# Kernel optimization log

Hardware: AMD Instinct MI355X
Metric: run time of the kernel (lower is better)

Reference implementation:

```python
import jax, jax.numpy as jnp
import numpy as np

NUM_HEADS = 4
ALPHA = 0.2  # LeakyReLU negative slope


def setup_inputs() -> dict:
    key = jax.random.key(0)
    k1, k2 = jax.random.split(key)
    input_tensor = jax.random.normal(k1, (2, 4096, 128), dtype=jnp.float32)
    adj_matrix = jax.random.randint(k2, (4096, 4096), 0, 2, dtype=jnp.int32)
    return {"input_tensor": input_tensor, "adj_matrix": adj_matrix}


def reference(input_tensor, adj_matrix):
    B, S, F = input_tensor.shape
    H = NUM_HEADS
    x = input_tensor.reshape(B, S, H, F // H)          # (B,S,H,K)
    # full dense score matrix, QK^T-like with shared projection (identity)
    scores = jnp.einsum('bihk,bjhk->bhij', x, x)        # (B,H,S,S)
    scores = jax.nn.leaky_relu(scores, negative_slope=ALPHA)
    # adjacency mask broadcast over (B,H)
    scores = jnp.where(adj_matrix[None, None, :, :] == 0, -jnp.inf, scores)
    probs = jax.nn.softmax(scores, axis=-1)             # dropout p=0 -> identity
    out = jnp.einsum('bhij,bjhk->bihk', probs, x)       # (B,S,H,K)
    return out.reshape(B, S, F)                          # concat=True
```

## Files before the change

### kernel.cpp

```cpp
#include <hip/hip_runtime.h>
#include <stdint.h>

#define SEQ 4096
#define FDIM 128
#define NH 4
#define HD 32
#define NB 2
#define NROWS (NB * NH * SEQ)
#define LOG2E 1.4426950408889634f
#define VCOL 72
#define VHALF (32 * VCOL)

typedef float f32x4 __attribute__((ext_vector_type(4)));
typedef float f32x2 __attribute__((ext_vector_type(2)));
typedef __bf16 bf16x8 __attribute__((ext_vector_type(8)));

__device__ __forceinline__ unsigned short f2bf(float f) {
  unsigned int u = __builtin_bit_cast(unsigned int, f);
  return (unsigned short)((u + 0x7FFFu + ((u >> 16) & 1u)) >> 16);
}

__global__ void cvt_kernel(const float* __restrict__ in, unsigned short* __restrict__ out) {
  int i = (blockIdx.x * 256 + threadIdx.x) * 4;
  float4 v = *reinterpret_cast<const float4*>(in + i);
  ushort4 o;
  o.x = f2bf(v.x); o.y = f2bf(v.y); o.z = f2bf(v.z); o.w = f2bf(v.w);
  *reinterpret_cast<ushort4*>(out + i) = o;
}

__global__ void adjpack_kernel(const int* __restrict__ adj, unsigned short* __restrict__ bits16) {
  size_t t = (size_t)blockIdx.x * 256 + threadIdx.x;
  const uint4* p = reinterpret_cast<const uint4*>(adj) + t * 4;
  uint4 a = p[0], b = p[1], c = p[2], d = p[3];
  unsigned m = 0;
  m |= (a.x != 0) ? 1u : 0u;        m |= (a.y != 0) ? 2u : 0u;
  m |= (a.z != 0) ? 4u : 0u;        m |= (a.w != 0) ? 8u : 0u;
  m |= (b.x != 0) ? 16u : 0u;       m |= (b.y != 0) ? 32u : 0u;
  m |= (b.z != 0) ? 64u : 0u;       m |= (b.w != 0) ? 128u : 0u;
  m |= (c.x != 0) ? 256u : 0u;      m |= (c.y != 0) ? 512u : 0u;
  m |= (c.z != 0) ? 1024u : 0u;     m |= (c.w != 0) ? 2048u : 0u;
  m |= (d.x != 0) ? 4096u : 0u;     m |= (d.y != 0) ? 8192u : 0u;
  m |= (d.z != 0) ? 16384u : 0u;    m |= (d.w != 0) ? 32768u : 0u;
  bits16[t] = (unsigned short)m;
}

#define STEP(T, RB, WBUF)                                                       \
  {                                                                             \
    __syncthreads();                                                            \
    const bool pfok = (T) + 1 < NT;                                             \
    if (pfok) {      \
      sptr += 64 * FDIM;                                                        \
      r0 = *reinterpret_cast<const uint2*>(sptr);                               \
      r1 = *reinterpret_cast<const uint2*>(sptr + FDIM);                        \
      wnext = brow[bcol0 + (T) + 1];                                            \
    }                                                                           \
    f32x4 sc[4];                                                                \
    __builtin_amdgcn_s_setprio(1);                                              \
    _Pragma("unroll") for (int t4 = 0; t4 < 4; ++t4) {                          \
      bf16x8 kf = __builtin_bit_cast(bf16x8,                                    \
          *reinterpret_cast<const uint4*>(&Kl[RB][t4 * 16 + ql][g * 8]));       \
      sc[t4] = __builtin_amdgcn_mfma_f32_16x16x32_bf16(kf, qf, zf, 0, 0, 0);    \
    }                                                                           \
    __builtin_amdgcn_s_setprio(0);                                              \
    const unsigned long long wsh = wcur >> (4 * g);                             \
    const int mwl = (int)(unsigned)wsh, mwh = (int)(unsigned)(wsh >> 32);       \
    float pf4[4][4];                                                            \
    _Pragma("unroll") for (int t4 = 0; t4 < 4; ++t4) {                          \
      const int word = (t4 & 2) ? mwh : mwl;                                    \
      f32x2 lo = {sc[t4][0], sc[t4][1]}, hi = {sc[t4][2], sc[t4][3]};           \
      f32x2 lo2, hi2;                                                           \
      asm("v_pk_mul_f32 %0, %1, %2" : "=v"(lo2) : "v"(lo), "v"(p02));           \
      asm("v_pk_mul_f32 %0, %1, %2" : "=v"(hi2) : "v"(hi), "v"(p02));           \
      _Pragma("unroll") for (int r = 0; r < 4; ++r) {                           \
        const float alt = (r < 2) ? lo2[r & 1] : hi2[r & 1];                    \
        const float v = fmaxf(sc[t4][r], alt);                  \
        const float e = __builtin_amdgcn_exp2f(v);          \
        const int msk = __builtin_amdgcn_sbfe(word, 16 * (t4 & 1) + r, 1);      \
        pf4[t4][r] = __builtin_bit_cast(                                        \
            float, __builtin_bit_cast(unsigned, e) & (unsigned)msk);            \
      }                                                                         \
    }                                                                           \
    __builtin_amdgcn_s_setprio(1);                                              \
    _Pragma("unroll") for (int u = 0; u < 2; ++u) {                             \
      bf16x8 pa;                                                                \
      _Pragma("unroll") for (int tp = 0; tp < 2; ++tp)                          \
          _Pragma("unroll") for (int r = 0; r < 4; ++r)                         \
              pa[tp * 4 + r] = (__bf16)pf4[2 * u + tp][r];                      \
      bf16x8 vf0 = __builtin_bit_cast(bf16x8,                                   \
          *reinterpret_cast<const uint4*>(&Vp[RB][ql * VCOL + u * 32 + g * 8]));        \
      bf16x8 vf1 = __builtin_bit_cast(bf16x8,                                   \
          *reinterpret_cast<const uint4*>(&Vp[RB][(16 + ql) * VCOL + u * 32 + g * 8])); \
      acc0 = __builtin_amdgcn_mfma_f32_16x16x32_bf16(pa, vf0, acc0, 0, 0, 0);   \
      acc1 = __builtin_amdgcn_mfma_f32_16x16x32_bf16(pa, vf1, acc1, 0, 0, 0);   \
      accL = __builtin_amdgcn_mfma_f32_16x16x32_bf16(pa, ones, accL, 0, 0, 0);  \
    }                                                                           \
    __builtin_amdgcn_s_setprio(0);                                              \
    if (pfok) {   \
      *reinterpret_cast<uint2*>(&Kl[WBUF][2 * pr][c4 * 4]) = r0;                \
      *reinterpret_cast<uint2*>(&Kl[WBUF][2 * pr + 1][c4 * 4]) = r1;            \
      unsigned* vw = reinterpret_cast<unsigned*>(&Vp[WBUF][0]) + pi0h;          \
      vw[(4 * c4 + 0) * 36] = __builtin_amdgcn_perm(r1.x, r0.x, selA);          \
      vw[(4 * c4 + 1) * 36] = __builtin_amdgcn_perm(r1.x, r0.x, selB);          \
      vw[(4 * c4 + 2) * 36] = __builtin_amdgcn_perm(r1.y, r0.y, selA);          \
      vw[(4 * c4 + 3) * 36] = __builtin_amdgcn_perm(r1.y, r0.y, selB);          \
    }                                                                           \
    wcur = wnext;                                                               \
  }

template <int NSPLIT>
__global__ __launch_bounds__(256, 4) void gat_kernel(
    const unsigned short* __restrict__ xbf,
    const unsigned long long* __restrict__ bits,
    float* __restrict__ dst,
    float* __restrict__ lbuf) {
  __shared__ __align__(16) unsigned short Kl[2][64][40];
  __shared__ __align__(16) unsigned short Vp[2][VHALF];

  const int bh = blockIdx.y;
  const int b = bh >> 2;
  const int h = bh & 3;
  const int tid = threadIdx.x;
  const int wid = tid >> 6;
  const int lane = tid & 63;
  const int g = lane >> 4;
  const int ql = lane & 15;
  const int qw = blockIdx.x * 64 + wid * 16;
  const int jbase = blockIdx.z * (SEQ / NSPLIT);
  const int NT = (SEQ / NSPLIT) / 64;

  const unsigned short* xb = xbf + ((size_t)b * SEQ) * FDIM + h * HD;

  bf16x8 qraw = __builtin_bit_cast(bf16x8,
      *reinterpret_cast<const uint4*>(xb + (size_t)(qw + ql) * FDIM + g * 8));
  bf16x8 qf;
#pragma unroll
  for (int e = 0; e < 8; ++e) qf[e] = (__bf16)((float)qraw[e] * LOG2E);

  bf16x8 ones;
#pragma unroll
  for (int e = 0; e < 8; ++e) ones[e] = (__bf16)1.0f;
  const f32x4 zf = {0.f, 0.f, 0.f, 0.f};
  const f32x2 p02 = {0.2f, 0.2f};

  f32x4 acc0 = {0.f, 0.f, 0.f, 0.f};
  f32x4 acc1 = {0.f, 0.f, 0.f, 0.f};
  f32x4 accL = {0.f, 0.f, 0.f, 0.f};

  const unsigned long long* brow = bits + (size_t)(qw + ql) * (SEQ / 64);
  const int bcol0 = jbase >> 6;

  const int pr = tid >> 3;
  const int c4 = tid & 7;
  const unsigned short* sptr = xb + (size_t)(jbase + 2 * pr) * FDIM + c4 * 4;

  const int pi0h =
      (32 * (pr >> 4) + 8 * ((pr >> 1) & 3) + 4 * ((pr >> 3) & 1) + 2 * (pr & 1)) >> 1;

  const unsigned selA = 0x05040100u;
  const unsigned selB = 0x07060302u;

  uint2 r0 = *reinterpret_cast<const uint2*>(sptr);
  uint2 r1 = *reinterpret_cast<const uint2*>(sptr + FDIM);
  unsigned long long wcur = brow[bcol0];
  unsigned long long wnext = 0;
  *reinterpret_cast<uint2*>(&Kl[0][2 * pr][c4 * 4]) = r0;
  *reinterpret_cast<uint2*>(&Kl[0][2 * pr + 1][c4 * 4]) = r1;
  {
    unsigned* vw = reinterpret_cast<unsigned*>(&Vp[0][0]) + pi0h;
    vw[(4 * c4 + 0) * 36] = __builtin_amdgcn_perm(r1.x, r0.x, selA);
    vw[(4 * c4 + 1) * 36] = __builtin_amdgcn_perm(r1.x, r0.x, selB);
    vw[(4 * c4 + 2) * 36] = __builtin_amdgcn_perm(r1.y, r0.y, selA);
    vw[(4 * c4 + 3) * 36] = __builtin_amdgcn_perm(r1.y, r0.y, selB);
  }

  for (int t = 0; t < NT; t += 2) {
    STEP(t, 0, 1);
    STEP(t + 1, 1, 0);
  }

  if (NSPLIT == 1) {
#pragma unroll
    for (int r = 0; r < 4; ++r) {
      const float inv = 1.f / accL[r];
      const size_t o = ((size_t)b * SEQ + (size_t)(qw + 4 * g + r)) * FDIM + h * HD;
      dst[o + ql] = acc0[r] * inv;
      dst[o + 16 + ql] = acc1[r] * inv;
    }
  } else {
    float* Op = dst + (((size_t)blockIdx.z * (NB * NH) + bh) * SEQ) * HD;
#pragma unroll
    for (int r = 0; r < 4; ++r) {
      const int q = qw + 4 * g + r;
      Op[(size_t)q * HD + ql] = acc0[r];
      Op[(size_t)q * HD + 16 + ql] = acc1[r];
    }
    if (ql == 0) {
#pragma unroll
      for (int r = 0; r < 4; ++r)
        lbuf[(size_t)blockIdx.z * NROWS + (size_t)bh * SEQ + qw + 4 * g + r] = accL[r];
    }
  }
}

template <int NSPLIT>
__global__ __launch_bounds__(256) void combine_kernel(
    const float* __restrict__ Op, const float* __restrict__ lbuf, float* __restrict__ out) {
  const int idx = blockIdx.x * 256 + threadIdx.x;
  const int row = idx >> 3;
  const int dc = (idx & 7) * 4;
  float lt = 0.f;
  float4 o = {0.f, 0.f, 0.f, 0.f};
#pragma unroll
  for (int s = 0; s < NSPLIT; ++s) {
    lt += lbuf[(size_t)s * NROWS + row];
    float4 v = *reinterpret_cast<const float4*>(Op + ((size_t)s * NROWS + row) * HD + dc);
    o.x += v.x; o.y += v.y; o.z += v.z; o.w += v.w;
  }
  const float inv = 1.f / lt;
  const int bh = row >> 12;
  const int q = row & (SEQ - 1);
  const int b = bh >> 2;
  const int h = bh & 3;
  float4 w;
  w.x = o.x * inv; w.y = o.y * inv; w.z = o.z * inv; w.w = o.w * inv;
  *reinterpret_cast<float4*>(out + ((size_t)b * SEQ + q) * FDIM + h * HD + dc) = w;
}

extern "C" void kernel_launch(void* const* d_in, const int* in_sizes, int n_in,
                              void* d_out, int out_size, void* d_ws, size_t ws_size,
                              hipStream_t stream) {
  (void)in_sizes; (void)n_in; (void)out_size;
  const float* x = (const float*)d_in[0];
  const int* adj = (const int*)d_in[1];
  float* outp = (float*)d_out;

  unsigned short* xbf = (unsigned short*)d_ws;
  unsigned short* bits16 = (unsigned short*)((char*)d_ws + (2u << 20));
  float* Opart = (float*)((char*)d_ws + (4u << 20));
  auto need = [](int s) {
    return (size_t)(4u << 20) + (size_t)s * NROWS * HD * 4 + (size_t)s * NROWS * 4;
  };

  cvt_kernel<<<(NB * SEQ * FDIM) / (256 * 4), 256, 0, stream>>>(x, xbf);
  adjpack_kernel<<<(SEQ * SEQ) / (16 * 256), 256, 0, stream>>>(adj, bits16);

  const unsigned long long* bits = (const unsigned long long*)bits16;
  if (ws_size >= need(4)) {
    float* mlb = (float*)((char*)d_ws + (4u << 20) + (size_t)4 * NROWS * HD * 4);
    dim3 grid(SEQ / 64, NB * NH, 4);
    gat_kernel<4><<<grid, 256, 0, stream>>>(xbf, bits, Opart, mlb);
    combine_kernel<4><<<(NROWS * 8) / 256, 256, 0, stream>>>(Opart, mlb, outp);
  } else if (ws_size >= need(2)) {
    float* mlb = (float*)((char*)d_ws + (4u << 20) + (size_t)2 * NROWS * HD * 4);
    dim3 grid(SEQ / 64, NB * NH, 2);
    gat_kernel<2><<<grid, 256, 0, stream>>>(xbf, bits, Opart, mlb);
    combine_kernel<2><<<(NROWS * 8) / 256, 256, 0, stream>>>(Opart, mlb, outp);
  } else {
    dim3 grid(SEQ / 64, NB * NH, 1);
    gat_kernel<1><<<grid, 256, 0, stream>>>(xbf, bits, outp, nullptr);
  }
}
```

Baseline: 75.88 us.

## Process two 16-query tiles per wave to reuse shared K/V fragments

Each wave now handles 32 query rows (two 16-row MFMA tiles) instead of 16, so every K and V fragment loaded from shared memory feeds twice as many MFMAs and the per-block staging of K/V tiles covers 128 queries. The grid shrinks by half in x. The leaky-relu is rewritten as a scalar fmaxf(v, 0.2v) instead of packed multiplies. The cost is roughly double accumulator and score registers per thread, which may lower occupancy under launch_bounds(256,4), and half as many blocks for the GPU to spread across its compute units.

Result: faster. 71.13 us (-6.3%).

```diff
diff --git a/kernel.cpp b/kernel.cpp
--- a/kernel.cpp
+++ b/kernel.cpp
@@ -12,7 +12,6 @@
 #define VHALF (32 * VCOL)
 
 typedef float f32x4 __attribute__((ext_vector_type(4)));
-typedef float f32x2 __attribute__((ext_vector_type(2)));
 typedef __bf16 bf16x8 __attribute__((ext_vector_type(8)));
 
 __device__ __forceinline__ unsigned short f2bf(float f) {
@@ -44,6 +43,29 @@
   bits16[t] = (unsigned short)m;
 }
 
+#define SOFTMAX_HALF(SC, WC, PA0, PA1)                                          \
+  {                                                                             \
+    const unsigned long long wsh = (WC) >> (4 * g);                             \
+    const int mwl = (int)(unsigned)wsh, mwh = (int)(unsigned)(wsh >> 32);       \
+    float pf4[4][4];                                                            \
+    _Pragma("unroll") for (int t4 = 0; t4 < 4; ++t4) {                          \
+      const int word = (t4 & 2) ? mwh : mwl;                                    \
+      _Pragma("unroll") for (int r = 0; r < 4; ++r) {                           \
+        float v = SC[t4][r];                                                    \
+        v = fmaxf(v, 0.2f * v);                                 \
+        float e = __builtin_amdgcn_exp2f(v);                \
+        const int msk = __builtin_amdgcn_sbfe(word, 16 * (t4 & 1) + r, 1);      \
+        pf4[t4][r] = __builtin_bit_cast(                                        \
+            float, __builtin_bit_cast(unsigned, e) & (unsigned)msk);            \
+      }                                                                         \
+    }                                                                           \
+    _Pragma("unroll") for (int tp = 0; tp < 2; ++tp)                            \
+        _Pragma("unroll") for (int r = 0; r < 4; ++r) {                         \
+          PA0[tp * 4 + r] = (__bf16)pf4[tp][r];                                 \
+          PA1[tp * 4 + r] = (__bf16)pf4[2 + tp][r];                             \
+        }                                                                       \
+  }
+
 #define STEP(T, RB, WBUF)                                                       \
   {                                                                             \
     __syncthreads();                                                            \
@@ -52,48 +74,45 @@
       sptr += 64 * FDIM;                                                        \
       r0 = *reinterpret_cast<const uint2*>(sptr);                               \
       r1 = *reinterpret_cast<const uint2*>(sptr + FDIM);                        \
-      wnext = brow[bcol0 + (T) + 1];                                            \
-    }                                                                           \
-    f32x4 sc[4];                                                                \
+      wnA = browA[bcol0 + (T) + 1];                                             \
+      wnB = browB[bcol0 + (T) + 1];                                             \
+    }                                                                           \
+                     \
+    bf16x8 kf[4];                                                               \
+    _Pragma("unroll") for (int t4 = 0; t4 < 4; ++t4)                            \
+        kf[t4] = __builtin_bit_cast(bf16x8,                                     \
+            *reinterpret_cast<const uint4*>(&Kl[RB][t4 * 16 + ql][g * 8]));     \
+    bf16x8 vf0 = __builtin_bit_cast(bf16x8,                                     \
+        *reinterpret_cast<const uint4*>(&Vp[RB][ql * VCOL + g * 8]));           \
+    bf16x8 vf1 = __builtin_bit_cast(bf16x8,                                     \
+        *reinterpret_cast<const uint4*>(&Vp[RB][(16 + ql) * VCOL + g * 8]));    \
+    bf16x8 vf2 = __builtin_bit_cast(bf16x8,                                     \
+        *reinterpret_cast<const uint4*>(&Vp[RB][ql * VCOL + 32 + g * 8]));      \
+    bf16x8 vf3 = __builtin_bit_cast(bf16x8,                                     \
+        *reinterpret_cast<const uint4*>(&Vp[RB][(16 + ql) * VCOL + 32 + g * 8])); \
+    f32x4 scA[4], scB[4];                                                       \
     __builtin_amdgcn_s_setprio(1);                                              \
     _Pragma("unroll") for (int t4 = 0; t4 < 4; ++t4) {                          \
-      bf16x8 kf = __builtin_bit_cast(bf16x8,                                    \
-          *reinterpret_cast<const uint4*>(&Kl[RB][t4 * 16 + ql][g * 8]));       \
-      sc[t4] = __builtin_amdgcn_mfma_f32_16x16x32_bf16(kf, qf, zf, 0, 0, 0);    \
+      scA[t4] = __builtin_amdgcn_mfma_f32_16x16x32_bf16(kf[t4], qfA, zf, 0, 0, 0); \
+      scB[t4] = __builtin_amdgcn_mfma_f32_16x16x32_bf16(kf[t4], qfB, zf, 0, 0, 0); \
     }                                                                           \
     __builtin_amdgcn_s_setprio(0);                                              \
-    const unsigned long long wsh = wcur >> (4 * g);                             \
-    const int mwl = (int)(unsigned)wsh, mwh = (int)(unsigned)(wsh >> 32);       \
-    float pf4[4][4];                                                            \
-    _Pragma("unroll") for (int t4 = 0; t4 < 4; ++t4) {                          \
-      const int word = (t4 & 2) ? mwh : mwl;                                    \
-      f32x2 lo = {sc[t4][0], sc[t4][1]}, hi = {sc[t4][2], sc[t4][3]};           \
-      f32x2 lo2, hi2;                                                           \
-      asm("v_pk_mul_f32 %0, %1, %2" : "=v"(lo2) : "v"(lo), "v"(p02));           \
-      asm("v_pk_mul_f32 %0, %1, %2" : "=v"(hi2) : "v"(hi), "v"(p02));           \
-      _Pragma("unroll") for (int r = 0; r < 4; ++r) {                           \
-        const float alt = (r < 2) ? lo2[r & 1] : hi2[r & 1];                    \
-        const float v = fmaxf(sc[t4][r], alt);                  \
-        const float e = __builtin_amdgcn_exp2f(v);          \
-        const int msk = __builtin_amdgcn_sbfe(word, 16 * (t4 & 1) + r, 1);      \
-        pf4[t4][r] = __builtin_bit_cast(                                        \
-            float, __builtin_bit_cast(unsigned, e) & (unsigned)msk);            \
-      }                                                                         \
-    }                                                                           \
+    bf16x8 paA0, paA1, paB0, paB1;                                              \
+    SOFTMAX_HALF(scA, wcA, paA0, paA1);                                         \
+    SOFTMAX_HALF(scB, wcB, paB0, paB1);                                         \
     __builtin_amdgcn_s_setprio(1);                                              \
-    _Pragma("unroll") for (int u = 0; u < 2; ++u) {                             \
-      bf16x8 pa;                                                                \
-      _Pragma("unroll") for (int tp = 0; tp < 2; ++tp)                          \
-          _Pragma("unroll") for (int r = 0; r < 4; ++r)                         \
-              pa[tp * 4 + r] = (__bf16)pf4[2 * u + tp][r];                      \
-      bf16x8 vf0 = __builtin_bit_cast(bf16x8,                                   \
-          *reinterpret_cast<const uint4*>(&Vp[RB][ql * VCOL + u * 32 + g * 8]));        \
-      bf16x8 vf1 = __builtin_bit_cast(bf16x8,                                   \
-          *reinterpret_cast<const uint4*>(&Vp[RB][(16 + ql) * VCOL + u * 32 + g * 8])); \
-      acc0 = __builtin_amdgcn_mfma_f32_16x16x32_bf16(pa, vf0, acc0, 0, 0, 0);   \
-      acc1 = __builtin_amdgcn_mfma_f32_16x16x32_bf16(pa, vf1, acc1, 0, 0, 0);   \
-      accL = __builtin_amdgcn_mfma_f32_16x16x32_bf16(pa, ones, accL, 0, 0, 0);  \
-    }                                                                           \
+    accA0 = __builtin_amdgcn_mfma_f32_16x16x32_bf16(paA0, vf0, accA0, 0, 0, 0); \
+    accA1 = __builtin_amdgcn_mfma_f32_16x16x32_bf16(paA0, vf1, accA1, 0, 0, 0); \
+    accLA = __builtin_amdgcn_mfma_f32_16x16x32_bf16(paA0, ones, accLA, 0, 0, 0);\
+    accA0 = __builtin_amdgcn_mfma_f32_16x16x32_bf16(paA1, vf2, accA0, 0, 0, 0); \
+    accA1 = __builtin_amdgcn_mfma_f32_16x16x32_bf16(paA1, vf3, accA1, 0, 0, 0); \
+    accLA = __builtin_amdgcn_mfma_f32_16x16x32_bf16(paA1, ones, accLA, 0, 0, 0);\
+    accB0 = __builtin_amdgcn_mfma_f32_16x16x32_bf16(paB0, vf0, accB0, 0, 0, 0); \
+    accB1 = __builtin_amdgcn_mfma_f32_16x16x32_bf16(paB0, vf1, accB1, 0, 0, 0); \
+    accLB = __builtin_amdgcn_mfma_f32_16x16x32_bf16(paB0, ones, accLB, 0, 0, 0);\
+    accB0 = __builtin_amdgcn_mfma_f32_16x16x32_bf16(paB1, vf2, accB0, 0, 0, 0); \
+    accB1 = __builtin_amdgcn_mfma_f32_16x16x32_bf16(paB1, vf3, accB1, 0, 0, 0); \
+    accLB = __builtin_amdgcn_mfma_f32_16x16x32_bf16(paB1, ones, accLB, 0, 0, 0);\
     __builtin_amdgcn_s_setprio(0);                                              \
     if (pfok) {   \
       *reinterpret_cast<uint2*>(&Kl[WBUF][2 * pr][c4 * 4]) = r0;                \
@@ -104,7 +123,8 @@
       vw[(4 * c4 + 2) * 36] = __builtin_amdgcn_perm(r1.y, r0.y, selA);          \
       vw[(4 * c4 + 3) * 36] = __builtin_amdgcn_perm(r1.y, r0.y, selB);          \
     }                                                                           \
-    wcur = wnext;                                                               \
+    wcA = wnA;                                                                  \
+    wcB = wnB;                                                                  \
   }
 
 template <int NSPLIT>
@@ -124,29 +144,35 @@
   const int lane = tid & 63;
   const int g = lane >> 4;
   const int ql = lane & 15;
-  const int qw = blockIdx.x * 64 + wid * 16;
+  const int qw = blockIdx.x * 128 + wid * 32;
   const int jbase = blockIdx.z * (SEQ / NSPLIT);
   const int NT = (SEQ / NSPLIT) / 64;
 
   const unsigned short* xb = xbf + ((size_t)b * SEQ) * FDIM + h * HD;
 
-  bf16x8 qraw = __builtin_bit_cast(bf16x8,
+  bf16x8 qrA = __builtin_bit_cast(bf16x8,
       *reinterpret_cast<const uint4*>(xb + (size_t)(qw + ql) * FDIM + g * 8));
-  bf16x8 qf;
-#pragma unroll
-  for (int e = 0; e < 8; ++e) qf[e] = (__bf16)((float)qraw[e] * LOG2E);
+  bf16x8 qrB = __builtin_bit_cast(bf16x8,
+      *reinterpret_cast<const uint4*>(xb + (size_t)(qw + 16 + ql) * FDIM + g * 8));
+  bf16x8 qfA, qfB;
+#pragma unroll
+  for (int e = 0; e < 8; ++e) {
+    qfA[e] = (__bf16)((float)qrA[e] * LOG2E);
+    qfB[e] = (__bf16)((float)qrB[e] * LOG2E);
+  }
 
   bf16x8 ones;
 #pragma unroll
   for (int e = 0; e < 8; ++e) ones[e] = (__bf16)1.0f;
   const f32x4 zf = {0.f, 0.f, 0.f, 0.f};
-  const f32x2 p02 = {0.2f, 0.2f};
-
-  f32x4 acc0 = {0.f, 0.f, 0.f, 0.f};
-  f32x4 acc1 = {0.f, 0.f, 0.f, 0.f};
-  f32x4 accL = {0.f, 0.f, 0.f, 0.f};
-
-  const unsigned long long* brow = bits + (size_t)(qw + ql) * (SEQ / 64);
+
+  f32x4 accA0 = {0.f, 0.f, 0.f, 0.f}, accA1 = {0.f, 0.f, 0.f, 0.f};
+  f32x4 accLA = {0.f, 0.f, 0.f, 0.f};
+  f32x4 accB0 = {0.f, 0.f, 0.f, 0.f}, accB1 = {0.f, 0.f, 0.f, 0.f};
+  f32x4 accLB = {0.f, 0.f, 0.f, 0.f};
+
+  const unsigned long long* browA = bits + (size_t)(qw + ql) * (SEQ / 64);
+  const unsigned long long* browB = bits + (size_t)(qw + 16 + ql) * (SEQ / 64);
   const int bcol0 = jbase >> 6;
 
   const int pr = tid >> 3;
@@ -161,8 +187,8 @@
 
   uint2 r0 = *reinterpret_cast<const uint2*>(sptr);
   uint2 r1 = *reinterpret_cast<const uint2*>(sptr + FDIM);
-  unsigned long long wcur = brow[bcol0];
-  unsigned long long wnext = 0;
+  unsigned long long wcA = browA[bcol0], wcB = browB[bcol0];
+  unsigned long long wnA = 0, wnB = 0;
   *reinterpret_cast<uint2*>(&Kl[0][2 * pr][c4 * 4]) = r0;
   *reinterpret_cast<uint2*>(&Kl[0][2 * pr + 1][c4 * 4]) = r1;
   {
@@ -181,23 +207,32 @@
   if (NSPLIT == 1) {
 #pragma unroll
     for (int r = 0; r < 4; ++r) {
-      const float inv = 1.f / accL[r];
-      const size_t o = ((size_t)b * SEQ + (size_t)(qw + 4 * g + r)) * FDIM + h * HD;
-      dst[o + ql] = acc0[r] * inv;
-      dst[o + 16 + ql] = acc1[r] * inv;
+      const float invA = 1.f / accLA[r];
+      const float invB = 1.f / accLB[r];
+      const size_t oA = ((size_t)b * SEQ + (size_t)(qw + 4 * g + r)) * FDIM + h * HD;
+      const size_t oB = ((size_t)b * SEQ + (size_t)(qw + 16 + 4 * g + r)) * FDIM + h * HD;
+      dst[oA + ql] = accA0[r] * invA;
+      dst[oA + 16 + ql] = accA1[r] * invA;
+      dst[oB + ql] = accB0[r] * invB;
+      dst[oB + 16 + ql] = accB1[r] * invB;
     }
   } else {
     float* Op = dst + (((size_t)blockIdx.z * (NB * NH) + bh) * SEQ) * HD;
 #pragma unroll
     for (int r = 0; r < 4; ++r) {
-      const int q = qw + 4 * g + r;
-      Op[(size_t)q * HD + ql] = acc0[r];
-      Op[(size_t)q * HD + 16 + ql] = acc1[r];
+      const int qA = qw + 4 * g + r;
+      const int qB = qw + 16 + 4 * g + r;
+      Op[(size_t)qA * HD + ql] = accA0[r];
+      Op[(size_t)qA * HD + 16 + ql] = accA1[r];
+      Op[(size_t)qB * HD + ql] = accB0[r];
+      Op[(size_t)qB * HD + 16 + ql] = accB1[r];
     }
     if (ql == 0) {
 #pragma unroll
-      for (int r = 0; r < 4; ++r)
-        lbuf[(size_t)blockIdx.z * NROWS + (size_t)bh * SEQ + qw + 4 * g + r] = accL[r];
+      for (int r = 0; r < 4; ++r) {
+        lbuf[(size_t)blockIdx.z * NROWS + (size_t)bh * SEQ + qw + 4 * g + r] = accLA[r];
+        lbuf[(size_t)blockIdx.z * NROWS + (size_t)bh * SEQ + qw + 16 + 4 * g + r] = accLB[r];
+      }
     }
   }
 }
@@ -247,16 +282,16 @@
   const unsigned long long* bits = (const unsigned long long*)bits16;
   if (ws_size >= need(4)) {
     float* mlb = (float*)((char*)d_ws + (4u << 20) + (size_t)4 * NROWS * HD * 4);
-    dim3 grid(SEQ / 64, NB * NH, 4);
+    dim3 grid(SEQ / 128, NB * NH, 4);
     gat_kernel<4><<<grid, 256, 0, stream>>>(xbf, bits, Opart, mlb);
     combine_kernel<4><<<(NROWS * 8) / 256, 256, 0, stream>>>(Opart, mlb, outp);
   } else if (ws_size >= need(2)) {
     float* mlb = (float*)((char*)d_ws + (4u << 20) + (size_t)2 * NROWS * HD * 4);
-    dim3 grid(SEQ / 64, NB * NH, 2);
+    dim3 grid(SEQ / 128, NB * NH, 2);
     gat_kernel<2><<<grid, 256, 0, stream>>>(xbf, bits, Opart, mlb);
     combine_kernel<2><<<(NROWS * 8) / 256, 256, 0, stream>>>(Opart, mlb, outp);
   } else {
-    dim3 grid(SEQ / 64, NB * NH, 1);
+    dim3 grid(SEQ / 128, NB * NH, 1);
     gat_kernel<1><<<grid, 256, 0, stream>>>(xbf, bits, outp, nullptr);
   }
 }
```
